# Optimization experiments

Measured on AMD Instinct MI355X. Metric: run time of the kernel, lower is better.

The kernel has to match this reference:

```python
import jax, jax.numpy as jnp
import numpy as np
from jax import lax

DEPTH_MAX = 6.0
NBINS = 100


def _minpool2d(x):
    # torch: -max_pool2d(-x, 5, 1, 2)  (max_pool pads with -inf => minpool pads with +inf)
    return lax.reduce_window(x, jnp.inf, lax.min, (1, 5, 5), (1, 1, 1),
                             [(0, 0), (2, 2), (2, 2)])


def _maxpool3d(x):
    return lax.reduce_window(x, -jnp.inf, lax.max, (1, 5, 5, 5), (1, 1, 1, 1),
                             [(0, 0), (2, 2), (2, 2), (2, 2)])


def _stuff_padding(row, maxvec):
    # fill zeros of `row` with the first nonzero element of `maxvec`
    v = maxvec[jnp.argmax(maxvec != 0)]  # if all-zero, argmax->0, v=0 (no-op fill)
    return jnp.where(row == 0, v, row)


def _find_none(a):
    # Sequential nearest-nonzero fill: for each zero (left->right), set it to
    # max(min nonzero on the left incl. previous fills, min nonzero on the right
    # of the ORIGINAL array). Expressed as a parallel suffix-min + lax.scan.
    aval = jnp.where(a != 0, a, jnp.inf)
    rev = lax.cummin(aval[::-1])[::-1]
    suf = jnp.concatenate([rev[1:], jnp.full((1,), jnp.inf, a.dtype)])  # min of a[i+1:]

    def step(m, xs):
        ai, si = xs
        l = jnp.where(jnp.isinf(m), 0.0, m)
        r = jnp.where(jnp.isinf(si), 0.0, si)
        val = jnp.where(ai == 0, jnp.maximum(l, r), ai)
        m = jnp.where(val != 0, jnp.minimum(m, val), m)
        return m, val

    _, out = lax.scan(step, jnp.array(jnp.inf, a.dtype), (a, suf))
    return out


def _forward(semantic2d, depth, occupancy2d, kept, mapping):
    B, K, H, W = semantic2d.shape
    D = kept.shape[1]
    sem = jnp.argmax(semantic2d, axis=1)               # [B,H,W]
    feats_sm = jax.nn.softmax(semantic2d, axis=1)      # [B,K,H,W]

    depth = lax.stop_gradient(depth)                   # pred['depth'].detach()
    depth = jnp.minimum(depth, DEPTH_MAX)              # clamp to depth_max
    depth_index = (depth / DEPTH_MAX * 100.0).astype(jnp.int32)  # [B,1,H,W]
    bins = jnp.arange(NBINS, dtype=jnp.int32)[None, :, None, None]

    # stuff mask: erosion (min-pool 5x5) of (semantic >= 10)
    stuff = _minpool2d((sem >= 10).astype(depth.dtype)) > 0.5    # [B,H,W] bool
    stuff_depth = depth[:, 0] * stuff                            # [B,H,W]
    stuff_x_max = stuff_depth.max(axis=1)                        # [B,W]
    stuff_y_max = stuff_depth.max(axis=2)                        # [B,H]

    pad_v = jax.vmap(_stuff_padding)
    sd = stuff_depth
    sd = sd.at[:, 0].set(pad_v(stuff_depth[:, 0], stuff_y_max))
    sd = sd.at[:, -1].set(pad_v(stuff_depth[:, -1], stuff_y_max[:, ::-1]))
    sd = sd.at[:, :, 0].set(pad_v(stuff_depth[:, :, 0], stuff_x_max))
    sd = sd.at[:, :, -1].set(pad_v(stuff_depth[:, :, -1], stuff_x_max[:, ::-1]))

    stuff_x = jax.vmap(_find_none)(sd.max(axis=1))   # [B,W]
    stuff_y = jax.vmap(_find_none)(sd.max(axis=2))   # [B,H]

    # per-pixel max depth: min(stuff_x[b, x], stuff_y[b, y])
    depth_max = jnp.minimum(stuff_x[:, None, None, :], stuff_y[:, None, :, None])  # [B,1,H,W]
    depth_max_bins = (depth_max / DEPTH_MAX * 100.0).astype(jnp.int32)

    depth_feat = (bins - depth_index).astype(depth.dtype) / 100.0 * DEPTH_MAX  # [B,100,H,W]
    depth_feat = jnp.stack([jnp.sign(depth_feat), jnp.abs(depth_feat)], axis=1)  # [B,2,100,H,W]

    depth_weight_kept = (bins > depth_index - 3) & (bins < depth_max_bins + 5)  # [B,100,H,W]
    depth_weight = jax.nn.sigmoid(occupancy2d) * depth_weight_kept

    # voxel -> pixel/bin gather: mapping columns are (batch, x, y, depth_m)
    b_idx = mapping[..., 0].astype(jnp.int32)
    x_idx = mapping[..., 1].astype(jnp.int32)
    y_idx = mapping[..., 2].astype(jnp.int32)
    d_idx = (mapping[..., 3] * 100.0 / DEPTH_MAX).astype(jnp.int32)
    feat_kept = kept & depth_weight_kept[b_idx, d_idx, y_idx, x_idx]  # [B,D,D,D]

    features = jnp.concatenate([
        jnp.broadcast_to(feats_sm[:, :, None], (B, K, NBINS, H, W)),
        depth_weight[:, None],
        depth_feat,
    ], axis=1)  # [B, K+3, 100, H, W]

    # padding voxels: dilation of feat_kept within kept, coords snapped to even
    padding_kept = (_maxpool3d(feat_kept.astype(jnp.float32)) > 0.5) & kept
    batch_point = padding_kept.reshape(B, -1).sum(-1)
    padding_kept = padding_kept.at[:, 127, 127, 127].set(
        jnp.where(batch_point == 0, True, padding_kept[:, 127, 127, 127]))
    padding_kept = padding_kept & ~feat_kept
    blocks = padding_kept.reshape(B, D // 2, 2, D // 2, 2, D // 2, 2).any(axis=(2, 4, 6))
    padding_even = jnp.zeros_like(padding_kept).at[:, ::2, ::2, ::2].set(blocks)

    union = feat_kept | padding_even          # occupied sparse coords (dense form)
    mask = _maxpool3d(union.astype(jnp.float32)) > 0.5
    return features, feat_kept, mask


def setup_inputs() -> dict:
    key = jax.random.key(0)
    ks = jax.random.split(key, 7)
    B, K, H, W, D = 2, 12, 120, 160, 128
    semantic2d = jax.random.normal(ks[0], (B, K, H, W), jnp.float32)
    depth = jax.random.uniform(ks[1], (B, 1, H, W), jnp.float32) * 8.0  # some > depth_max
    occupancy2d = jax.random.normal(ks[2], (B, 100, H, W), jnp.float32)
    kept = jax.random.uniform(ks[3], (B, D, D, D)) < 0.05
    b_col = jnp.broadcast_to(jnp.arange(B, dtype=jnp.float32)[:, None, None, None], (B, D, D, D))
    x_col = jax.random.randint(ks[4], (B, D, D, D), 0, W).astype(jnp.float32)
    y_col = jax.random.randint(ks[5], (B, D, D, D), 0, H).astype(jnp.float32)
    d_col = jax.random.uniform(ks[6], (B, D, D, D)) * (DEPTH_MAX - 1e-3)
    mapping = jnp.stack([b_col, x_col, y_col, d_col], axis=-1)  # [B,D,D,D,4]
    return {"semantic2d": semantic2d, "depth": depth, "occupancy2d": occupancy2d,
            "kept": kept, "mapping": mapping}


def reference(semantic2d, depth, occupancy2d, kept, mapping):
    return _forward(semantic2d, depth, occupancy2d, kept, mapping)
```

## Files before the change

### kernel.cpp

```cpp
#include <hip/hip_runtime.h>
#include <cmath>

#define BB 2
#define KK 12
#define HH 120
#define WW 160
#define HW (HH*WW)
#define DD 128
#define NB 100
#define DMAXF 6.0f
#define NLINES (BB*DD*DD)
#define NVOX (BB*DD*DD*DD)
#define SDP 161

__global__ void k1_pixel(const float* __restrict__ sem2d, const float* __restrict__ depth,
                         float* __restrict__ feats_sm, float* __restrict__ stuffflag,
                         int* __restrict__ di_arr) {
    int t = blockIdx.x * blockDim.x + threadIdx.x;
    if (t >= BB * HW) return;
    int b = t / HW, p = t - b * HW;
    const float* sp = sem2d + (size_t)b * KK * HW + p;
    float v[KK];
    float mx = -INFINITY; int am = 0;
#pragma unroll
    for (int k = 0; k < KK; k++) {
        v[k] = sp[(size_t)k * HW];
        if (v[k] > mx) { mx = v[k]; am = k; }
    }
    float s = 0.f;
#pragma unroll
    for (int k = 0; k < KK; k++) { v[k] = expf(v[k] - mx); s += v[k]; }
    float inv = 1.f / s;
    float* fp = feats_sm + (size_t)b * KK * HW + p;
#pragma unroll
    for (int k = 0; k < KK; k++) fp[(size_t)k * HW] = v[k] * inv;
    stuffflag[t] = (am >= 10) ? 1.f : 0.f;
    float d = fminf(depth[t], DMAXF);
    di_arr[t] = (int)((d / DMAXF) * 100.0f);
}

__global__ __launch_bounds__(256) void k23_stuff(const float* __restrict__ stuffflag,
                                                 const float* __restrict__ depth,
                                                 int* __restrict__ dmb_arr) {
    __shared__ float sd[HH * SDP];
    __shared__ unsigned int bA[600];
    __shared__ unsigned int bB[600];
    __shared__ float ymax[HH], xmax[WW], colmax[WW], rowmax[HH];
    __shared__ float sufc[WW], sufr[HH];
    __shared__ float sxv[WW], syv[HH];
    __shared__ float vv[4];
    int b = blockIdx.x, t = threadIdx.x;
    const float* sf = stuffflag + b * HW;
    const float* dp = depth + b * HW;

    for (int it = 0; it < HW / 256; ++it) {
        int p = it * 256 + t;
        bool fl = sf[p] > 0.5f;
        unsigned long long m = __ballot(fl);
        int lane = t & 63;
        if (lane == 0)  bA[p >> 5] = (unsigned int)m;
        if (lane == 32) bA[p >> 5] = (unsigned int)(m >> 32);
    }
    __syncthreads();

    for (int q = t; q < 600; q += 256) {
        int w = q % 5;
        unsigned int cur = bA[q];
        unsigned int left  = (w > 0) ? bA[q - 1] : 0xFFFFFFFFu;
        unsigned int right = (w < 4) ? bA[q + 1] : 0xFFFFFFFFu;
        unsigned int sL1 = (cur >> 1) | (right << 31);
        unsigned int sL2 = (cur >> 2) | (right << 30);
        unsigned int sR1 = (cur << 1) | (left >> 31);
        unsigned int sR2 = (cur << 2) | (left >> 30);
        bB[q] = cur & sL1 & sL2 & sR1 & sR2;
    }
    __syncthreads();

    for (int q = t; q < 600; q += 256) {
        int h = q / 5, w = q - h * 5;
        unsigned int v = 0xFFFFFFFFu;
#pragma unroll
        for (int dh = -2; dh <= 2; ++dh) {
            int hh = h + dh;
            if (hh >= 0 && hh < HH) v &= bB[hh * 5 + w];
        }
        bA[q] = v;
    }
    __syncthreads();

    for (int it = 0; it < HW / 256; ++it) {
        int p = it * 256 + t;
        int h = p / WW, w = p - h * WW;
        unsigned int bit = (bA[p >> 5] >> (p & 31)) & 1u;
        float d = fminf(dp[p], DMAXF);
        sd[h * SDP + w] = bit ? d : 0.f;
    }
    __syncthreads();

    if (t < HH) { float m = -INFINITY; for (int w = 0; w < WW; w++) m = fmaxf(m, sd[t * SDP + w]); ymax[t] = m; }
    if (t < WW) { float m = -INFINITY; for (int h = 0; h < HH; h++) m = fmaxf(m, sd[h * SDP + t]); xmax[t] = m; }
    __syncthreads();

    if (t == 0) {
        float f = 0.f, l = 0.f;
        for (int h = 0; h < HH; h++) { if (ymax[h] != 0.f) { f = ymax[h]; break; } }
        for (int h = HH - 1; h >= 0; h--) { if (ymax[h] != 0.f) { l = ymax[h]; break; } }
        vv[0] = f; vv[1] = l;
    }
    if (t == 1) {
        float f = 0.f, l = 0.f;
        for (int w = 0; w < WW; w++) { if (xmax[w] != 0.f) { f = xmax[w]; break; } }
        for (int w = WW - 1; w >= 0; w--) { if (xmax[w] != 0.f) { l = xmax[w]; break; } }
        vv[2] = f; vv[3] = l;
    }
    __syncthreads();
    float v1 = vv[0], v2 = vv[1], v3 = vv[2], v4 = vv[3];

    auto sdval = [&](int h, int w) -> float {
        float x = sd[h * SDP + w];
        if (w == 0)      return (x == 0.f) ? v3 : x;
        if (w == WW - 1) return (x == 0.f) ? v4 : x;
        if (h == 0)      return (x == 0.f) ? v1 : x;
        if (h == HH - 1) return (x == 0.f) ? v2 : x;
        return x;
    };
    if (t < WW) { float m = -INFINITY; for (int h = 0; h < HH; h++) m = fmaxf(m, sdval(h, t)); colmax[t] = m; }
    if (t < HH) { float m = -INFINITY; for (int w = 0; w < WW; w++) m = fmaxf(m, sdval(t, w)); rowmax[t] = m; }
    __syncthreads();

    if (t == 0) {
        float m = INFINITY;
        for (int i = WW - 1; i >= 0; i--) { sufc[i] = m; float a = colmax[i]; if (a != 0.f) m = fminf(m, a); }
        m = INFINITY;
        for (int i = 0; i < WW; i++) {
            float a = colmax[i];
            float l = (m == INFINITY) ? 0.f : m;
            float r = (sufc[i] == INFINITY) ? 0.f : sufc[i];
            float val = (a == 0.f) ? fmaxf(l, r) : a;
            if (val != 0.f) m = fminf(m, val);
            sxv[i] = val;
        }
    }
    if (t == 1) {
        float m = INFINITY;
        for (int i = HH - 1; i >= 0; i--) { sufr[i] = m; float a = rowmax[i]; if (a != 0.f) m = fminf(m, a); }
        m = INFINITY;
        for (int i = 0; i < HH; i++) {
            float a = rowmax[i];
            float l = (m == INFINITY) ? 0.f : m;
            float r = (sufr[i] == INFINITY) ? 0.f : sufr[i];
            float val = (a == 0.f) ? fmaxf(l, r) : a;
            if (val != 0.f) m = fminf(m, val);
            syv[i] = val;
        }
    }
    __syncthreads();

    for (int it = 0; it < HW / 256; ++it) {
        int p = it * 256 + t;
        int h = p / WW, w = p - h * WW;
        float dm = fminf(sxv[w], syv[h]);
        dmb_arr[b * HW + p] = (int)((dm / DMAXF) * 100.0f);
    }
}

__device__ inline void comp1(float o, int di, int db, int bin, float& dw, float& sg, float& ad) {
    bool dwk = (bin > di - 3) && (bin < db + 5);
    float s = 1.f / (1.f + __expf(-o));
    dw = dwk ? s : 0.f;
    float df = ((float)(bin - di)) / 100.0f * DMAXF;
    sg = (float)((bin > di) - (bin < di));
    ad = fabsf(df);
}

__global__ void k4_features(const float4* __restrict__ occ4, const float4* __restrict__ fs4,
                            const int4* __restrict__ di4, const int4* __restrict__ dmb4,
                            float4* __restrict__ out4) {
    const int HW4 = HW / 4;
    int t = blockIdx.x * blockDim.x + threadIdx.x;
    if (t >= BB * NB * HW4) return;
    int b = t / (NB * HW4);
    int r = t - b * (NB * HW4);
    int bin = r / HW4;
    int p4 = r - bin * HW4;
    int4 di = di4[b * HW4 + p4];
    int4 db = dmb4[b * HW4 + p4];
    float4 o = occ4[t];
    float4 dw, sgn, adf;
    comp1(o.x, di.x, db.x, bin, dw.x, sgn.x, adf.x);
    comp1(o.y, di.y, db.y, bin, dw.y, sgn.y, adf.y);
    comp1(o.z, di.z, db.z, bin, dw.z, sgn.z, adf.z);
    comp1(o.w, di.w, db.w, bin, dw.w, sgn.w, adf.w);
    size_t base = (size_t)(b * 15 * NB + bin) * HW4 + p4;
    const float4* fp = fs4 + (size_t)b * KK * HW4 + p4;
#pragma unroll
    for (int c = 0; c < KK; c++) out4[base + (size_t)c * NB * HW4] = fp[(size_t)c * HW4];
    out4[base + (size_t)12 * NB * HW4] = dw;
    out4[base + (size_t)13 * NB * HW4] = sgn;
    out4[base + (size_t)14 * NB * HW4] = adf;
}

__global__ void k5_gather(const int* __restrict__ kept, const float4* __restrict__ mapping,
                          const int* __restrict__ di_arr, const int* __restrict__ dmb_arr,
                          float* __restrict__ out_fk, unsigned int* __restrict__ fk_pk,
                          unsigned int* __restrict__ kept_pk) {
    int v = blockIdx.x * blockDim.x + threadIdx.x;
    float4 m = mapping[v];
    int bi = (int)m.x, xi = (int)m.y, yi = (int)m.z;
    int dIdx = (int)((m.w * 100.0f) / DMAXF);
    int kp = kept[v];
    int pp = bi * HW + yi * WW + xi;
    int di = di_arr[pp], db = dmb_arr[pp];
    bool dwk = (dIdx > di - 3) && (dIdx < db + 5);
    bool fk = (kp != 0) && dwk;
    out_fk[v] = fk ? 1.f : 0.f;
    unsigned long long mb = __ballot(fk);
    unsigned long long mk = __ballot(kp != 0);
    int lane = threadIdx.x & 63;
    if (lane == 0)  { fk_pk[v >> 5] = (unsigned int)mb;         kept_pk[v >> 5] = (unsigned int)mk; }
    if (lane == 32) { fk_pk[v >> 5] = (unsigned int)(mb >> 32); kept_pk[v >> 5] = (unsigned int)(mk >> 32); }
}

__device__ inline void kdil128(unsigned int w0, unsigned int w1, unsigned int w2, unsigned int w3,
                               unsigned int* r) {
    unsigned int a0 = w0, a1 = w1, a2 = w2, a3 = w3;
    a0 |= w0 << 1; a1 |= (w1 << 1) | (w0 >> 31); a2 |= (w2 << 1) | (w1 >> 31); a3 |= (w3 << 1) | (w2 >> 31);
    a0 |= w0 << 2; a1 |= (w1 << 2) | (w0 >> 30); a2 |= (w2 << 2) | (w1 >> 30); a3 |= (w3 << 2) | (w2 >> 30);
    a0 |= (w0 >> 1) | (w1 << 31); a1 |= (w1 >> 1) | (w2 << 31); a2 |= (w2 >> 1) | (w3 << 31); a3 |= w3 >> 1;
    a0 |= (w0 >> 2) | (w1 << 30); a1 |= (w1 >> 2) | (w2 << 30); a2 |= (w2 >> 2) | (w3 << 30); a3 |= w3 >> 2;
    r[0] = a0; r[1] = a1; r[2] = a2; r[3] = a3;
}

__global__ void k6_dil_jk(const uint4* __restrict__ in, uint4* __restrict__ outb,
                          int* __restrict__ counters) {
    int l = blockIdx.x * blockDim.x + threadIdx.x;
    if (l == 0) { counters[0] = 0; counters[1] = 0; }
    int b = l / (DD * DD); int rem = l - b * DD * DD; int i = rem / DD; int j = rem - i * DD;
    unsigned int a0 = 0, a1 = 0, a2 = 0, a3 = 0;
#pragma unroll
    for (int dj = -2; dj <= 2; dj++) {
        int jj = j + dj; if (jj < 0 || jj >= DD) continue;
        uint4 x = in[(b * DD + i) * DD + jj];
        a0 |= x.x; a1 |= x.y; a2 |= x.z; a3 |= x.w;
    }
    unsigned int r[4];
    kdil128(a0, a1, a2, a3, r);
    outb[l] = make_uint4(r[0], r[1], r[2], r[3]);
}

__global__ void k7_dil_i_count(const uint4* __restrict__ tmp1, const uint4* __restrict__ kept_pk,
                               uint4* __restrict__ pad0, int* __restrict__ counters) {
    int l = blockIdx.x * blockDim.x + threadIdx.x;
    int b = l / (DD * DD); int rem = l - b * DD * DD; int i = rem / DD; int j = rem - i * DD;
    unsigned int a0 = 0, a1 = 0, a2 = 0, a3 = 0;
#pragma unroll
    for (int di = -2; di <= 2; di++) {
        int ii = i + di; if (ii < 0 || ii >= DD) continue;
        uint4 x = tmp1[(b * DD + ii) * DD + j];
        a0 |= x.x; a1 |= x.y; a2 |= x.z; a3 |= x.w;
    }
    uint4 kk = kept_pk[l];
    a0 &= kk.x; a1 &= kk.y; a2 &= kk.z; a3 &= kk.w;
    pad0[l] = make_uint4(a0, a1, a2, a3);
    unsigned long long bal = __ballot((a0 | a1 | a2 | a3) != 0u);
    if ((threadIdx.x & 63) == 0 && bal) atomicOr(&counters[b], 1);
}

__global__ void k8ab_union(const uint4* __restrict__ pad0, const uint4* __restrict__ fk_pk,
                           const int* __restrict__ counters, uint4* __restrict__ uni) {
    int l = blockIdx.x * blockDim.x + threadIdx.x;
    int b = l >> 14; int rem = l & 16383; int i = rem >> 7; int j = rem & 127;
    uint4 u = fk_pk[l];
    if (((i | j) & 1) == 0) {
        bool c0 = (counters[b] == 0);
        unsigned int q0 = 0, q1 = 0, q2 = 0, q3 = 0;
#pragma unroll
        for (int di2 = 0; di2 < 2; di2++)
#pragma unroll
            for (int dj2 = 0; dj2 < 2; dj2++) {
                int ii = i + di2, jj = j + dj2;
                int ll = (b * DD + ii) * DD + jj;
                uint4 p = pad0[ll]; uint4 f = fk_pk[ll];
                unsigned int pw = p.w;
                if (c0 && ii == 127 && jj == 127) pw |= 0x80000000u;
                q0 |= p.x & ~f.x; q1 |= p.y & ~f.y; q2 |= p.z & ~f.z; q3 |= pw & ~f.w;
            }
        q0 = (q0 | (q0 >> 1)) & 0x55555555u;
        q1 = (q1 | (q1 >> 1)) & 0x55555555u;
        q2 = (q2 | (q2 >> 1)) & 0x55555555u;
        q3 = (q3 | (q3 >> 1)) & 0x55555555u;
        u.x |= q0; u.y |= q1; u.z |= q2; u.w |= q3;
    }
    uni[l] = u;
}

__global__ void k11f_dil_unpack(const unsigned int* __restrict__ tmp1w, float4* __restrict__ outm) {
    int t = blockIdx.x * blockDim.x + threadIdx.x;
    int vb = t << 2;
    int line = vb >> 7;
    int wi = (vb >> 5) & 3;
    int bo = vb & 31;
    int b = line >> 14; int rem = line & 16383; int i = rem >> 7; int j = rem & 127;
    unsigned int w = 0;
#pragma unroll
    for (int di = -2; di <= 2; di++) {
        int ii = i + di;
        if (ii >= 0 && ii < DD) w |= tmp1w[((b * DD + ii) * DD + j) * 4 + wi];
    }
    float4 r;
    r.x = (float)((w >> bo) & 1u);
    r.y = (float)((w >> (bo + 1)) & 1u);
    r.z = (float)((w >> (bo + 2)) & 1u);
    r.w = (float)((w >> (bo + 3)) & 1u);
    outm[t] = r;
}

extern "C" void kernel_launch(void* const* d_in, const int* in_sizes, int n_in,
                              void* d_out, int out_size, void* d_ws, size_t ws_size,
                              hipStream_t stream) {
    (void)in_sizes; (void)n_in; (void)out_size; (void)ws_size;
    const float* sem2d   = (const float*)d_in[0];
    const float* depth   = (const float*)d_in[1];
    const float* occ     = (const float*)d_in[2];
    const int*   kept    = (const int*)d_in[3];
    const float* mapping = (const float*)d_in[4];
    float* out = (float*)d_out;

    float* feats_sm    = (float*)d_ws;
    float* stuffflag   = feats_sm + BB * KK * HW;
    int*   di_arr      = (int*)(stuffflag + BB * HW);
    int*   dmb_arr     = di_arr + BB * HW;
    unsigned int* fk_pk   = (unsigned int*)(dmb_arr + BB * HW);
    unsigned int* kept_pk = fk_pk + NVOX / 32;
    unsigned int* tmp1    = kept_pk + NVOX / 32;
    unsigned int* pad0    = tmp1 + NVOX / 32;
    unsigned int* uni     = pad0 + NVOX / 32;
    int* counters = (int*)(uni + NVOX / 32);

    k1_pixel<<<BB * HW / 256, 256, 0, stream>>>(sem2d, depth, feats_sm, stuffflag, di_arr);
    k23_stuff<<<BB, 256, 0, stream>>>(stuffflag, depth, dmb_arr);

    k4_features<<<BB * NB * (HW / 4) / 256, 256, 0, stream>>>(
        (const float4*)occ, (const float4*)feats_sm, (const int4*)di_arr, (const int4*)dmb_arr,
        (float4*)out);

    k5_gather<<<NVOX / 256, 256, 0, stream>>>(kept, (const float4*)mapping, di_arr, dmb_arr,
                                              out + (size_t)57600000, fk_pk, kept_pk);

    int lineBlocks = NLINES / 256;
    k6_dil_jk<<<lineBlocks, 256, 0, stream>>>((const uint4*)fk_pk, (uint4*)tmp1, counters);
    k7_dil_i_count<<<lineBlocks, 256, 0, stream>>>((const uint4*)tmp1, (const uint4*)kept_pk,
                                                   (uint4*)pad0, counters);
    k8ab_union<<<lineBlocks, 256, 0, stream>>>((const uint4*)pad0, (const uint4*)fk_pk, counters,
                                               (uint4*)uni);
    k6_dil_jk<<<lineBlocks, 256, 0, stream>>>((const uint4*)uni, (uint4*)tmp1, counters);
    k11f_dil_unpack<<<NVOX / 4 / 256, 256, 0, stream>>>(tmp1, (float4*)(out + (size_t)61794304));
}
```

Before: 521.3 us.

## Fuse feature/gather launches and merge voxel dilation passes into LDS slab kernels

Merges the feature-expansion kernel and the voxel gather kernel into one launch that splits work by block index. It also replaces the separate dilation, pad, union and unpack kernels with two slab kernels. These stage 32-row slabs plus halo rows in shared memory and do the j/k and i dilations there, avoiding global temporaries and several launches. The cost is that the slab kernels run on only BB*4 blocks of 512 threads with large LDS footprints. The final mask unpack, which writes a large output, is therefore serialized over very few CUs, with a high risk of losing memory bandwidth parallelism.

```diff
diff --git a/kernel.cpp b/kernel.cpp
--- a/kernel.cpp
+++ b/kernel.cpp
@@ -12,6 +12,7 @@
 #define NLINES (BB*DD*DD)
 #define NVOX (BB*DD*DD*DD)
 #define SDP 161
+#define SLAB 32
 
 __global__ void k1_pixel(const float* __restrict__ sem2d, const float* __restrict__ depth,
                          float* __restrict__ feats_sm, float* __restrict__ stuffflag,
@@ -173,52 +174,55 @@
     ad = fabsf(df);
 }
 
-__global__ void k4_features(const float4* __restrict__ occ4, const float4* __restrict__ fs4,
-                            const int4* __restrict__ di4, const int4* __restrict__ dmb4,
-                            float4* __restrict__ out4) {
-    const int HW4 = HW / 4;
-    int t = blockIdx.x * blockDim.x + threadIdx.x;
-    if (t >= BB * NB * HW4) return;
-    int b = t / (NB * HW4);
-    int r = t - b * (NB * HW4);
-    int bin = r / HW4;
-    int p4 = r - bin * HW4;
-    int4 di = di4[b * HW4 + p4];
-    int4 db = dmb4[b * HW4 + p4];
-    float4 o = occ4[t];
-    float4 dw, sgn, adf;
-    comp1(o.x, di.x, db.x, bin, dw.x, sgn.x, adf.x);
-    comp1(o.y, di.y, db.y, bin, dw.y, sgn.y, adf.y);
-    comp1(o.z, di.z, db.z, bin, dw.z, sgn.z, adf.z);
-    comp1(o.w, di.w, db.w, bin, dw.w, sgn.w, adf.w);
-    size_t base = (size_t)(b * 15 * NB + bin) * HW4 + p4;
-    const float4* fp = fs4 + (size_t)b * KK * HW4 + p4;
-#pragma unroll
-    for (int c = 0; c < KK; c++) out4[base + (size_t)c * NB * HW4] = fp[(size_t)c * HW4];
-    out4[base + (size_t)12 * NB * HW4] = dw;
-    out4[base + (size_t)13 * NB * HW4] = sgn;
-    out4[base + (size_t)14 * NB * HW4] = adf;
-}
-
-__global__ void k5_gather(const int* __restrict__ kept, const float4* __restrict__ mapping,
-                          const int* __restrict__ di_arr, const int* __restrict__ dmb_arr,
-                          float* __restrict__ out_fk, unsigned int* __restrict__ fk_pk,
-                          unsigned int* __restrict__ kept_pk) {
-    int v = blockIdx.x * blockDim.x + threadIdx.x;
-    float4 m = mapping[v];
-    int bi = (int)m.x, xi = (int)m.y, yi = (int)m.z;
-    int dIdx = (int)((m.w * 100.0f) / DMAXF);
-    int kp = kept[v];
-    int pp = bi * HW + yi * WW + xi;
-    int di = di_arr[pp], db = dmb_arr[pp];
-    bool dwk = (dIdx > di - 3) && (dIdx < db + 5);
-    bool fk = (kp != 0) && dwk;
-    out_fk[v] = fk ? 1.f : 0.f;
-    unsigned long long mb = __ballot(fk);
-    unsigned long long mk = __ballot(kp != 0);
-    int lane = threadIdx.x & 63;
-    if (lane == 0)  { fk_pk[v >> 5] = (unsigned int)mb;         kept_pk[v >> 5] = (unsigned int)mk; }
-    if (lane == 32) { fk_pk[v >> 5] = (unsigned int)(mb >> 32); kept_pk[v >> 5] = (unsigned int)(mk >> 32); }
+#define FEAT_BLOCKS (BB * NB * (HW/4) / 256)
+
+__global__ void k45_feat_gather(const float4* __restrict__ occ4, const float4* __restrict__ fs4,
+                                const int4* __restrict__ di4, const int4* __restrict__ dmb4,
+                                float4* __restrict__ out4,
+                                const int* __restrict__ kept, const float4* __restrict__ mapping,
+                                const int* __restrict__ di_arr, const int* __restrict__ dmb_arr,
+                                float* __restrict__ out_fk, unsigned int* __restrict__ fk_pk,
+                                unsigned int* __restrict__ kept_pk, int* __restrict__ counters) {
+    if (blockIdx.x < FEAT_BLOCKS) {
+        const int HW4 = HW / 4;
+        int t = blockIdx.x * blockDim.x + threadIdx.x;
+        int b = t / (NB * HW4);
+        int r = t - b * (NB * HW4);
+        int bin = r / HW4;
+        int p4 = r - bin * HW4;
+        int4 di = di4[b * HW4 + p4];
+        int4 db = dmb4[b * HW4 + p4];
+        float4 o = occ4[t];
+        float4 dw, sgn, adf;
+        comp1(o.x, di.x, db.x, bin, dw.x, sgn.x, adf.x);
+        comp1(o.y, di.y, db.y, bin, dw.y, sgn.y, adf.y);
+        comp1(o.z, di.z, db.z, bin, dw.z, sgn.z, adf.z);
+        comp1(o.w, di.w, db.w, bin, dw.w, sgn.w, adf.w);
+        size_t base = (size_t)(b * 15 * NB + bin) * HW4 + p4;
+        const float4* fp = fs4 + (size_t)b * KK * HW4 + p4;
+#pragma unroll
+        for (int c = 0; c < KK; c++) out4[base + (size_t)c * NB * HW4] = fp[(size_t)c * HW4];
+        out4[base + (size_t)12 * NB * HW4] = dw;
+        out4[base + (size_t)13 * NB * HW4] = sgn;
+        out4[base + (size_t)14 * NB * HW4] = adf;
+    } else {
+        int v = (blockIdx.x - FEAT_BLOCKS) * blockDim.x + threadIdx.x;
+        if (v == 0) { counters[0] = 0; counters[1] = 0; }
+        float4 m = mapping[v];
+        int bi = (int)m.x, xi = (int)m.y, yi = (int)m.z;
+        int dIdx = (int)((m.w * 100.0f) / DMAXF);
+        int kp = kept[v];
+        int pp = bi * HW + yi * WW + xi;
+        int di = di_arr[pp], db = dmb_arr[pp];
+        bool dwk = (dIdx > di - 3) && (dIdx < db + 5);
+        bool fk = (kp != 0) && dwk;
+        out_fk[v] = fk ? 1.f : 0.f;
+        unsigned long long mb = __ballot(fk);
+        unsigned long long mk = __ballot(kp != 0);
+        int lane = threadIdx.x & 63;
+        if (lane == 0)  { fk_pk[v >> 5] = (unsigned int)mb;         kept_pk[v >> 5] = (unsigned int)mk; }
+        if (lane == 32) { fk_pk[v >> 5] = (unsigned int)(mb >> 32); kept_pk[v >> 5] = (unsigned int)(mk >> 32); }
+    }
 }
 
 __device__ inline void kdil128(unsigned int w0, unsigned int w1, unsigned int w2, unsigned int w3,
@@ -231,88 +235,138 @@
     r[0] = a0; r[1] = a1; r[2] = a2; r[3] = a3;
 }
 
-__global__ void k6_dil_jk(const uint4* __restrict__ in, uint4* __restrict__ outb,
-                          int* __restrict__ counters) {
-    int l = blockIdx.x * blockDim.x + threadIdx.x;
-    if (l == 0) { counters[0] = 0; counters[1] = 0; }
-    int b = l / (DD * DD); int rem = l - b * DD * DD; int i = rem / DD; int j = rem - i * DD;
-    unsigned int a0 = 0, a1 = 0, a2 = 0, a3 = 0;
-#pragma unroll
-    for (int dj = -2; dj <= 2; dj++) {
-        int jj = j + dj; if (jj < 0 || jj >= DD) continue;
-        uint4 x = in[(b * DD + i) * DD + jj];
-        a0 |= x.x; a1 |= x.y; a2 |= x.z; a3 |= x.w;
-    }
-    unsigned int r[4];
-    kdil128(a0, a1, a2, a3, r);
-    outb[l] = make_uint4(r[0], r[1], r[2], r[3]);
-}
-
-__global__ void k7_dil_i_count(const uint4* __restrict__ tmp1, const uint4* __restrict__ kept_pk,
-                               uint4* __restrict__ pad0, int* __restrict__ counters) {
-    int l = blockIdx.x * blockDim.x + threadIdx.x;
-    int b = l / (DD * DD); int rem = l - b * DD * DD; int i = rem / DD; int j = rem - i * DD;
-    unsigned int a0 = 0, a1 = 0, a2 = 0, a3 = 0;
-#pragma unroll
-    for (int di = -2; di <= 2; di++) {
-        int ii = i + di; if (ii < 0 || ii >= DD) continue;
-        uint4 x = tmp1[(b * DD + ii) * DD + j];
-        a0 |= x.x; a1 |= x.y; a2 |= x.z; a3 |= x.w;
-    }
-    uint4 kk = kept_pk[l];
-    a0 &= kk.x; a1 &= kk.y; a2 &= kk.z; a3 &= kk.w;
-    pad0[l] = make_uint4(a0, a1, a2, a3);
-    unsigned long long bal = __ballot((a0 | a1 | a2 | a3) != 0u);
-    if ((threadIdx.x & 63) == 0 && bal) atomicOr(&counters[b], 1);
-}
-
-__global__ void k8ab_union(const uint4* __restrict__ pad0, const uint4* __restrict__ fk_pk,
-                           const int* __restrict__ counters, uint4* __restrict__ uni) {
-    int l = blockIdx.x * blockDim.x + threadIdx.x;
-    int b = l >> 14; int rem = l & 16383; int i = rem >> 7; int j = rem & 127;
-    uint4 u = fk_pk[l];
-    if (((i | j) & 1) == 0) {
-        bool c0 = (counters[b] == 0);
-        unsigned int q0 = 0, q1 = 0, q2 = 0, q3 = 0;
-#pragma unroll
-        for (int di2 = 0; di2 < 2; di2++)
-#pragma unroll
-            for (int dj2 = 0; dj2 < 2; dj2++) {
-                int ii = i + di2, jj = j + dj2;
-                int ll = (b * DD + ii) * DD + jj;
-                uint4 p = pad0[ll]; uint4 f = fk_pk[ll];
-                unsigned int pw = p.w;
-                if (c0 && ii == 127 && jj == 127) pw |= 0x80000000u;
-                q0 |= p.x & ~f.x; q1 |= p.y & ~f.y; q2 |= p.z & ~f.z; q3 |= pw & ~f.w;
-            }
-        q0 = (q0 | (q0 >> 1)) & 0x55555555u;
-        q1 = (q1 | (q1 >> 1)) & 0x55555555u;
-        q2 = (q2 | (q2 >> 1)) & 0x55555555u;
-        q3 = (q3 | (q3 >> 1)) & 0x55555555u;
-        u.x |= q0; u.y |= q1; u.z |= q2; u.w |= q3;
-    }
-    uni[l] = u;
-}
-
-__global__ void k11f_dil_unpack(const unsigned int* __restrict__ tmp1w, float4* __restrict__ outm) {
-    int t = blockIdx.x * blockDim.x + threadIdx.x;
-    int vb = t << 2;
-    int line = vb >> 7;
-    int wi = (vb >> 5) & 3;
-    int bo = vb & 31;
-    int b = line >> 14; int rem = line & 16383; int i = rem >> 7; int j = rem & 127;
-    unsigned int w = 0;
-#pragma unroll
-    for (int di = -2; di <= 2; di++) {
-        int ii = i + di;
-        if (ii >= 0 && ii < DD) w |= tmp1w[((b * DD + ii) * DD + j) * 4 + wi];
-    }
-    float4 r;
-    r.x = (float)((w >> bo) & 1u);
-    r.y = (float)((w >> (bo + 1)) & 1u);
-    r.z = (float)((w >> (bo + 2)) & 1u);
-    r.w = (float)((w >> (bo + 3)) & 1u);
-    outm[t] = r;
+__global__ __launch_bounds__(512) void kA_pad(const uint4* __restrict__ fk_pk,
+                                              const uint4* __restrict__ kept_pk,
+                                              uint4* __restrict__ pad0, int* __restrict__ counters) {
+    __shared__ uint4 fkS[SLAB + 4][DD];
+    __shared__ uint4 jkS[SLAB + 4][DD];
+    int b = blockIdx.x / (DD / SLAB);
+    int i0 = (blockIdx.x % (DD / SLAB)) * SLAB;
+    int t = threadIdx.x;
+
+    for (int q = t; q < (SLAB + 4) * DD; q += 512) {
+        int r = q >> 7, j = q & 127;
+        int gi = i0 - 2 + r;
+        uint4 v = make_uint4(0, 0, 0, 0);
+        if (gi >= 0 && gi < DD) v = fk_pk[(b * DD + gi) * DD + j];
+        fkS[r][j] = v;
+    }
+    __syncthreads();
+
+    for (int q = t; q < (SLAB + 4) * DD; q += 512) {
+        int r = q >> 7, j = q & 127;
+        unsigned int a0 = 0, a1 = 0, a2 = 0, a3 = 0;
+#pragma unroll
+        for (int dj = -2; dj <= 2; dj++) {
+            int jj = j + dj; if (jj < 0 || jj >= DD) continue;
+            uint4 x = fkS[r][jj];
+            a0 |= x.x; a1 |= x.y; a2 |= x.z; a3 |= x.w;
+        }
+        unsigned int rr[4]; kdil128(a0, a1, a2, a3, rr);
+        jkS[r][j] = make_uint4(rr[0], rr[1], rr[2], rr[3]);
+    }
+    __syncthreads();
+
+    unsigned int any = 0;
+    for (int q = t; q < SLAB * DD; q += 512) {
+        int r = (q >> 7) + 2, j = q & 127;
+        int gi = i0 + (q >> 7);
+        unsigned int a0 = 0, a1 = 0, a2 = 0, a3 = 0;
+#pragma unroll
+        for (int di = -2; di <= 2; di++) {
+            uint4 x = jkS[r + di][j];
+            a0 |= x.x; a1 |= x.y; a2 |= x.z; a3 |= x.w;
+        }
+        uint4 kk = kept_pk[(b * DD + gi) * DD + j];
+        a0 &= kk.x; a1 &= kk.y; a2 &= kk.z; a3 &= kk.w;
+        pad0[(b * DD + gi) * DD + j] = make_uint4(a0, a1, a2, a3);
+        any |= a0 | a1 | a2 | a3;
+    }
+    unsigned long long bal = __ballot(any != 0);
+    if ((t & 63) == 0 && bal) atomicOr(&counters[b], 1);
+}
+
+__global__ __launch_bounds__(512) void kB_mask(const uint4* __restrict__ pad0,
+                                               const uint4* __restrict__ fk_pk,
+                                               const int* __restrict__ counters,
+                                               float4* __restrict__ outm) {
+    __shared__ uint4 padS[SLAB + 5][DD];
+    __shared__ uint4 fkS[SLAB + 5][DD];
+    int b = blockIdx.x / (DD / SLAB);
+    int i0 = (blockIdx.x % (DD / SLAB)) * SLAB;
+    int t = threadIdx.x;
+    bool c0 = (counters[b] == 0);
+
+    for (int q = t; q < (SLAB + 5) * DD; q += 512) {
+        int r = q >> 7, j = q & 127;
+        int gi = i0 - 2 + r;
+        uint4 p = make_uint4(0, 0, 0, 0), f = make_uint4(0, 0, 0, 0);
+        if (gi >= 0 && gi < DD) {
+            p = pad0[(b * DD + gi) * DD + j];
+            f = fk_pk[(b * DD + gi) * DD + j];
+            if (c0 && gi == 127 && j == 127) p.w |= 0x80000000u;
+        }
+        padS[r][j] = p; fkS[r][j] = f;
+    }
+    __syncthreads();
+
+    for (int q = t; q < (SLAB + 4) * DD; q += 512) {
+        int r = q >> 7, j = q & 127;
+        int gi = i0 - 2 + r;
+        if (gi >= 0 && ((gi | j) & 1) == 0) {
+            unsigned int q0 = 0, q1 = 0, q2 = 0, q3 = 0;
+#pragma unroll
+            for (int di2 = 0; di2 < 2; di2++)
+#pragma unroll
+                for (int dj2 = 0; dj2 < 2; dj2++) {
+                    uint4 p = padS[r + di2][j + dj2];
+                    uint4 f = fkS[r + di2][j + dj2];
+                    q0 |= p.x & ~f.x; q1 |= p.y & ~f.y; q2 |= p.z & ~f.z; q3 |= p.w & ~f.w;
+                }
+            q0 = (q0 | (q0 >> 1)) & 0x55555555u;
+            q1 = (q1 | (q1 >> 1)) & 0x55555555u;
+            q2 = (q2 | (q2 >> 1)) & 0x55555555u;
+            q3 = (q3 | (q3 >> 1)) & 0x55555555u;
+            uint4 u = fkS[r][j];
+            u.x |= q0; u.y |= q1; u.z |= q2; u.w |= q3;
+            fkS[r][j] = u;
+        }
+    }
+    __syncthreads();
+
+    for (int q = t; q < (SLAB + 4) * DD; q += 512) {
+        int r = q >> 7, j = q & 127;
+        unsigned int a0 = 0, a1 = 0, a2 = 0, a3 = 0;
+#pragma unroll
+        for (int dj = -2; dj <= 2; dj++) {
+            int jj = j + dj; if (jj < 0 || jj >= DD) continue;
+            uint4 x = fkS[r][jj];
+            a0 |= x.x; a1 |= x.y; a2 |= x.z; a3 |= x.w;
+        }
+        unsigned int rr[4]; kdil128(a0, a1, a2, a3, rr);
+        padS[r][j] = make_uint4(rr[0], rr[1], rr[2], rr[3]);
+    }
+    __syncthreads();
+
+    for (int q = t; q < SLAB * DD * 32; q += 512) {
+        int c = q & 31;
+        int line = q >> 5;
+        int ioff = line >> 7, j = line & 127;
+        int r = ioff + 2;
+        int wi = c >> 3, bo = (c & 7) * 4;
+        unsigned int w = 0;
+#pragma unroll
+        for (int di = -2; di <= 2; di++) {
+            const unsigned int* pw = (const unsigned int*)&padS[r + di][j];
+            w |= pw[wi];
+        }
+        float4 o;
+        o.x = (float)((w >> bo) & 1u);
+        o.y = (float)((w >> (bo + 1)) & 1u);
+        o.z = (float)((w >> (bo + 2)) & 1u);
+        o.w = (float)((w >> (bo + 3)) & 1u);
+        outm[((size_t)((b * DD + (i0 + ioff)) * DD + j) * DD >> 2) + c] = o;
+    }
 }
 
 extern "C" void kernel_launch(void* const* d_in, const int* in_sizes, int n_in,
@@ -332,27 +386,20 @@
     int*   dmb_arr     = di_arr + BB * HW;
     unsigned int* fk_pk   = (unsigned int*)(dmb_arr + BB * HW);
     unsigned int* kept_pk = fk_pk + NVOX / 32;
-    unsigned int* tmp1    = kept_pk + NVOX / 32;
-    unsigned int* pad0    = tmp1 + NVOX / 32;
-    unsigned int* uni     = pad0 + NVOX / 32;
-    int* counters = (int*)(uni + NVOX / 32);
+    unsigned int* pad0    = kept_pk + NVOX / 32;
+    int* counters = (int*)(pad0 + NVOX / 32);
 
     k1_pixel<<<BB * HW / 256, 256, 0, stream>>>(sem2d, depth, feats_sm, stuffflag, di_arr);
     k23_stuff<<<BB, 256, 0, stream>>>(stuffflag, depth, dmb_arr);
 
-    k4_features<<<BB * NB * (HW / 4) / 256, 256, 0, stream>>>(
+    k45_feat_gather<<<FEAT_BLOCKS + NVOX / 256, 256, 0, stream>>>(
         (const float4*)occ, (const float4*)feats_sm, (const int4*)di_arr, (const int4*)dmb_arr,
-        (float4*)out);
-
-    k5_gather<<<NVOX / 256, 256, 0, stream>>>(kept, (const float4*)mapping, di_arr, dmb_arr,
-                                              out + (size_t)57600000, fk_pk, kept_pk);
-
-    int lineBlocks = NLINES / 256;
-    k6_dil_jk<<<lineBlocks, 256, 0, stream>>>((const uint4*)fk_pk, (uint4*)tmp1, counters);
-    k7_dil_i_count<<<lineBlocks, 256, 0, stream>>>((const uint4*)tmp1, (const uint4*)kept_pk,
-                                                   (uint4*)pad0, counters);
-    k8ab_union<<<lineBlocks, 256, 0, stream>>>((const uint4*)pad0, (const uint4*)fk_pk, counters,
-                                               (uint4*)uni);
-    k6_dil_jk<<<lineBlocks, 256, 0, stream>>>((const uint4*)uni, (uint4*)tmp1, counters);
-    k11f_dil_unpack<<<NVOX / 4 / 256, 256, 0, stream>>>(tmp1, (float4*)(out + (size_t)61794304));
-}
+        (float4*)out,
+        kept, (const float4*)mapping, di_arr, dmb_arr,
+        out + (size_t)57600000, fk_pk, kept_pk, counters);
+
+    kA_pad<<<BB * (DD / SLAB), 512, 0, stream>>>((const uint4*)fk_pk, (const uint4*)kept_pk,
+                                                 (uint4*)pad0, counters);
+    kB_mask<<<BB * (DD / SLAB), 512, 0, stream>>>((const uint4*)pad0, (const uint4*)fk_pk,
+                                                  counters, (float4*)(out + (size_t)61794304));
+}
```

Measured after the change: 551.8 us. +5.9%, slower.
